# Optimization experiments

Measured on AMD Instinct MI355X. Metric: run time of the kernel, lower is better.

Reference implementation:

```python
import jax, jax.numpy as jnp
import numpy as np

SEQ_LEN = 512
NUM_FEATURES = 16
BATCH = 8
D_MODEL = 512
TOP_K = 5
MAX_P = 512  # largest patch size == seq_len
LAMBD = 0.01


def get_patch_sizes(seq_len):
    # torch: 1/rfftfreq(L)[1:], floor, unique (desc), [::-1] -> ascending unique periods
    freqs = np.fft.rfftfreq(seq_len)[1:]
    periods = np.floor(1.0 / freqs).astype(np.int64)
    return [int(p) for p in np.unique(periods)]


def _sinusoid(n, d):
    pos = np.arange(n, dtype=np.float64)[:, None]
    i = np.arange(d, dtype=np.float64)[None, :]
    angle = pos / np.power(10000.0, (2.0 * np.floor(i / 2.0)) / d)
    return np.where((np.arange(d)[None, :] % 2) == 0, np.sin(angle), np.cos(angle))


def pos_emb_2d(d_model, C, N):
    # 2D sinusoidal positional embedding over (feature idx, patch idx):
    # first half of d_model encodes the feature dim, second half the patch position.
    half = d_model // 2
    pe_feat = _sinusoid(C, half)              # [C, half]
    pe_pos = _sinusoid(N, d_model - half)     # [N, d_model-half]
    pe = np.concatenate([
        np.broadcast_to(pe_feat[:, None, :], (C, N, half)),
        np.broadcast_to(pe_pos[None, :, :], (C, N, d_model - half)),
    ], axis=-1)
    return jnp.asarray(pe, dtype=jnp.float32)  # [C, N, d_model]


def softshrink(x, lambd=LAMBD):
    return jnp.where(x > lambd, x - lambd, jnp.where(x < -lambd, x + lambd, jnp.zeros_like(x)))


def _forward(x, w_start, b_start, w1, b1, w2, b2, w_gate, Wv):
    B, L, C = x.shape
    patch_sizes = get_patch_sizes(L)
    # ---- AFNO1D gating (eval mode: clean logits, no noise) ----
    xs = (x @ w_start)[..., 0] + b_start[0]           # start_fc -> [B, L]
    xf = jnp.fft.rfft(xs, norm='ortho')[:, 1:]        # drop DC -> [B, F], F = L//2
    xr, xi = jnp.real(xf), jnp.imag(xf)
    o1r = jax.nn.relu(xr @ w1[0] - xi @ w1[1] + b1[0])
    o1i = jax.nn.relu(xi @ w1[0] + xr @ w1[1] + b1[1])
    o2r = softshrink(o1r @ w2[0] - o1i @ w2[1] + b2[0])
    o2i = softshrink(o1i @ w2[0] + o1r @ w2[1] + b2[1])
    amp = jnp.sqrt(o2r * o2r + o2i * o2i + 1e-12)     # |complex|, eps for grad safety at 0
    logits = amp @ w_gate                             # [B, E]
    top_w, top_i = jax.lax.top_k(logits, TOP_K)
    top_w = jax.nn.softmax(top_w, axis=-1)
    gates = jnp.zeros_like(logits).at[jnp.arange(B)[:, None], top_i].set(top_w)
    # ---- per-patch-size embedding (dense dispatch: unrouted rows zeroed) ----
    xt = jnp.swapaxes(x, 1, 2)                        # [B, C, L]
    outs = []
    for i, p in enumerate(patch_sizes):               # static loop over 43 experts
        n = -(-L // p)                                # ceil(L / p)
        xp = jnp.pad(xt, ((0, 0), (0, 0), (0, n * p - L)), mode='edge')  # ReplicationPad1d
        patches = xp.reshape(B, C, n, p)              # unfold(-1, p, p)
        emb = jnp.einsum('bcnp,pd->bcnd', patches, Wv[i, :p, :])
        emb = emb + pos_emb_2d(D_MODEL, C, n)[None]
        mask = (gates[:, i] > 0).astype(emb.dtype)
        outs.append(emb * mask[:, None, None, None])
    emb_all = jnp.concatenate(outs, axis=2)           # [B, C, total_patches, d_model]
    return emb_all, gates


def setup_inputs():
    key = jax.random.key(0)
    ks = jax.random.split(key, 8)
    L, C, D = SEQ_LEN, NUM_FEATURES, D_MODEL
    F = L // 2
    E = len(get_patch_sizes(L))
    scale = 1.0 / D
    x = jax.random.normal(ks[0], (BATCH, L, C), jnp.float32)
    w_start = jax.random.normal(ks[1], (C, 1), jnp.float32) / float(np.sqrt(C))
    b_start = jnp.zeros((1,), jnp.float32)
    w1 = scale * jax.random.normal(ks[2], (2, F, 4 * F), jnp.float32)
    b1 = scale * jax.random.normal(ks[3], (2, 4 * F), jnp.float32)
    w2 = scale * jax.random.normal(ks[4], (2, 4 * F, F), jnp.float32)
    b2 = scale * jax.random.normal(ks[5], (2, F), jnp.float32)
    w_gate = 0.01 * jax.random.normal(ks[6], (F, E), jnp.float32)  # randn (not zeros) for nontrivial routing
    Wv = jax.random.normal(ks[7], (E, MAX_P, D), jnp.float32) / float(np.sqrt(MAX_P))  # padded per-expert Linear(p, d_model) weights; expert i uses Wv[i, :p_i]
    return {"x": x, "w_start": w_start, "b_start": b_start, "w1": w1, "b1": b1,
            "w2": w2, "b2": b2, "w_gate": w_gate, "Wv": Wv}


def reference(x, w_start, b_start, w1, b1, w2, b2, w_gate, Wv):
    return _forward(x, w_start, b_start, w1, b1, w2, b2, w_gate, Wv)
```

## Files before the change

### kernel.cpp

```cpp
#include <hip/hip_runtime.h>
#include <math.h>


typedef float v4f __attribute__((ext_vector_type(4)));

constexpr int NEXP = 43;
constexpr int NTOT = 1657;
constexpr long long GATES_OFF = 108593152LL;
constexpr int OUT_V4 = 27148288;

constexpr int WS_XR  = 0;
constexpr int WS_XI  = 2048;
constexpr int WS_O1R = 4096;
constexpr int WS_O1I = 12288;
constexpr int WS_P2  = 20480;
constexpr int WS_PEF = 53248;
constexpr int WS_PEP = 57344;

struct Tables {
  int P[NEXP], N[NEXP], SP[NEXP], G0[NEXP], T0[NEXP+1], TB[5], ne;
};
constexpr int split_of(int p) { return p >= 170 ? 8 : p >= 102 ? 4 : p >= 64 ? 2 : 1; }

constexpr Tables make_tables() {
  Tables t{};
  int ne = 0;
  for (int p = 2; p <= 512; ++p) {
    int k = 512 / p;
    if (k >= 1 && 512 / k == p) t.P[ne++] = p;
  }
  t.ne = ne;
  int g = 0, tl = 0;
  for (int i = 0; i < ne; ++i) {
    int p = t.P[i], n = (512 + p - 1) / p;
    t.N[i] = n; t.SP[i] = split_of(p);
    t.G0[i] = g;  g += n;
    t.T0[i] = tl; tl += n * t.SP[i];
  }
  t.T0[ne] = tl;
  t.TB[0] = 0;
  for (int l = 0; l < 4; ++l) {
    int s = (l == 0) ? 1 : (l == 1) ? 2 : (l == 2) ? 4 : 8;
    int a = 0;
    for (int i = 0; i < ne; ++i) if (t.SP[i] <= s) a += t.N[i] * t.SP[i];
    t.TB[l + 1] = a;
  }
  return t;
}
constexpr Tables HTBL = make_tables();
static_assert(HTBL.ne == 43, "expert count");
static_assert(HTBL.G0[42] + HTBL.N[42] == NTOT, "total patches");
static_assert(HTBL.T0[43] == 1759, "total tiles");
static_assert(HTBL.TB[4] == 1759, "boundaries");

constexpr int NTILE = 1759;
struct TileMap { int v[NTILE]; };
constexpr TileMap make_tmap() {
  TileMap tm{};
  int idx = 0;
  for (int i = 0; i < HTBL.ne; ++i)
    for (int m = 0; m < HTBL.N[i]; ++m)
      for (int cg = 0; cg < HTBL.SP[i]; ++cg)
        tm.v[idx++] = i | (m << 6) | (cg << 15);
  return tm;
}
__constant__ TileMap TMAPC = make_tmap();
__constant__ Tables  TBLC  = make_tables();

__global__ void k_pre(const float* __restrict__ x, const float* __restrict__ w_start,
                      const float* __restrict__ b_start, float* __restrict__ ws) {
  if (blockIdx.x < 8) {
    __shared__ float xs[512];
    int b = blockIdx.x, t = threadIdx.x;
    float w[16];
#pragma unroll
    for (int c = 0; c < 16; ++c) w[c] = w_start[c];
    float bs = b_start[0];
    for (int l = t; l < 512; l += 256) {
      const float* xp = x + ((size_t)b * 512 + l) * 16;
      float s = bs;
#pragma unroll
      for (int c = 0; c < 16; ++c) s = fmaf(xp[c], w[c], s);
      xs[l] = s;
    }
    __syncthreads();
    int k = t + 1;
    float ar = 0.f, ai = 0.f;
    int ph = 0;
    for (int l = 0; l < 512; ++l) {
      float a = (float)ph * (1.0f / 256.0f);
      float v = xs[l];
      ar = fmaf(v,  cospif(a), ar);
      ai = fmaf(-v, sinpif(a), ai);
      ph = (ph + k) & 511;
    }
    const float sc = 0.044194173824159216f;
    ws[WS_XR + b * 256 + t] = ar * sc;
    ws[WS_XI + b * 256 + t] = ai * sc;
  } else {
    int idx = (blockIdx.x - 8) * 256 + threadIdx.x;
    const float K = 0.03597789207803197f;
    if (idx < 4096) {
      int c = idx >> 8, d = idx & 255;
      float ang = (float)c * expf(-(float)(d & ~1) * K);
      ws[WS_PEF + idx] = (d & 1) ? cosf(ang) : sinf(ang);
    } else {
      int r = idx - 4096, mm = r >> 8, j = r & 255;
      float ang = (float)mm * expf(-(float)(j & ~1) * K);
      ws[WS_PEP + r] = (j & 1) ? cosf(ang) : sinf(ang);
    }
  }
}

__global__ void k_fc1(const float* __restrict__ w1, const float* __restrict__ b1,
                      float* __restrict__ ws) {
  __shared__ float xr[256], xi[256];
  int b = blockIdx.x >> 2, jg = blockIdx.x & 3, t = threadIdx.x;
  xr[t] = ws[WS_XR + b * 256 + t];
  xi[t] = ws[WS_XI + b * 256 + t];
  __syncthreads();
  int j = jg * 256 + t;
  float s_ra = 0.f, s_rb = 0.f, s_ia = 0.f, s_ib = 0.f;
  for (int k = 0; k < 256; ++k) {
    float a  = w1[k * 1024 + j];
    float bb = w1[262144 + k * 1024 + j];
    float r = xr[k], im = xi[k];
    s_ra = fmaf(r, a, s_ra);  s_ib = fmaf(im, bb, s_ib);
    s_ia = fmaf(im, a, s_ia); s_rb = fmaf(r, bb, s_rb);
  }
  ws[WS_O1R + b * 1024 + j] = fmaxf(s_ra - s_ib + b1[j], 0.f);
  ws[WS_O1I + b * 1024 + j] = fmaxf(s_ia + s_rb + b1[1024 + j], 0.f);
}

__global__ void k_fc2a(const float* __restrict__ w2, float* __restrict__ ws) {
  __shared__ float lr[256], li[256];
  int b = blockIdx.x >> 2, kc = blockIdx.x & 3, t = threadIdx.x;
  lr[t] = ws[WS_O1R + b * 1024 + kc * 256 + t];
  li[t] = ws[WS_O1I + b * 1024 + kc * 256 + t];
  __syncthreads();
  float s_rr = 0.f, s_ri = 0.f, s_ir = 0.f, s_ii = 0.f;
  int kb = kc * 256;
  for (int k = 0; k < 256; ++k) {
    float a  = w2[(kb + k) * 256 + t];
    float bb = w2[262144 + (kb + k) * 256 + t];
    float r = lr[k], im = li[k];
    s_rr = fmaf(r, a, s_rr);  s_ii = fmaf(im, bb, s_ii);
    s_ir = fmaf(im, a, s_ir); s_ri = fmaf(r, bb, s_ri);
  }
  float* P = ws + WS_P2 + (size_t)(b * 4 + kc) * 1024 + t;
  P[0] = s_rr; P[256] = s_ii; P[512] = s_ir; P[768] = s_ri;
}

__device__ __forceinline__ float softshrink(float v) {
  const float l = 0.01f;
  return v > l ? v - l : (v < -l ? v + l : 0.f);
}

__global__ void k_fc2b(const float* __restrict__ b2, const float* __restrict__ w_gate,
                       float* __restrict__ ws, float* __restrict__ out) {
  __shared__ float amp[256], lg[64];
  int b = blockIdx.x, t = threadIdx.x;
  float s_rr = 0.f, s_ii = 0.f, s_ir = 0.f, s_ri = 0.f;
  for (int kc = 0; kc < 4; ++kc) {
    const float* P = ws + WS_P2 + (size_t)(b * 4 + kc) * 1024 + t;
    s_rr += P[0]; s_ii += P[256]; s_ir += P[512]; s_ri += P[768];
  }
  float o2r = softshrink(s_rr - s_ii + b2[t]);
  float o2i = softshrink(s_ir + s_ri + b2[256 + t]);
  amp[t] = sqrtf(o2r * o2r + o2i * o2i + 1e-12f);
  __syncthreads();
  if (t < NEXP) {
    float s = 0.f;
    for (int k = 0; k < 256; ++k) s = fmaf(amp[k], w_gate[k * NEXP + t], s);
    lg[t] = s;
  }
  __syncthreads();
  if (t == 0) {
    float v[NEXP];
    for (int e = 0; e < NEXP; ++e) v[e] = lg[e];
    float vals[5]; int idx[5];
    for (int r = 0; r < 5; ++r) {
      float best = -INFINITY; int bi = 0;
      for (int e = 0; e < NEXP; ++e)
        if (v[e] > best) { best = v[e]; bi = e; }
      vals[r] = best; idx[r] = bi; v[bi] = -INFINITY;
    }
    float den = 0.f, wv[5];
    for (int r = 0; r < 5; ++r) { wv[r] = expf(vals[r] - vals[0]); den += wv[r]; }
    float g[NEXP];
    for (int e = 0; e < NEXP; ++e) g[e] = 0.f;
    for (int r = 0; r < 5; ++r) g[idx[r]] = wv[r] / den;
    for (int e = 0; e < NEXP; ++e) out[GATES_OFF + (size_t)b * NEXP + e] = g[e];
  }
}

__global__ void k_fill(float* __restrict__ out) {
  size_t id = (size_t)blockIdx.x * 256 + threadIdx.x;
  v4f z = {0.f, 0.f, 0.f, 0.f};
  v4f* o = (v4f*)out;
#pragma unroll
  for (int s = 0; s < 8; ++s)
    o[id + (size_t)s * 3393536] = z;
}

template <int CPG>
__global__ __launch_bounds__(256)
void k_embed(const float* __restrict__ x, const float* __restrict__ Wv,
             const float* __restrict__ ws, float* __restrict__ out, int base) {
  constexpr int CPT = CPG / 2;
  __shared__ __align__(16) float xl[1024];
  int tile = base + blockIdx.x, b = blockIdx.y, t = threadIdx.x;
  int info = TMAPC.v[tile];
  int i = info & 63, m = (info >> 6) & 511, cg = info >> 15;

  float gate = out[GATES_OFF + (size_t)b * NEXP + i];
  if (gate <= 0.f) return;

  int p  = TBLC.P[i];
  int c0 = cg * CPG;
  int g  = TBLC.G0[i] + m;
  int dg = t & 127, tch = t >> 7;
  int d0 = dg * 4;

  int tot = p * CPG;
  for (int id = t; id < tot; id += 256) {
    int q = id / CPG, cc = id % CPG;
    int l = m * p + q; l = l > 511 ? 511 : l;
    xl[id] = x[((size_t)b * 512 + l) * 16 + c0 + cc];
  }
  __syncthreads();

  v4f acc[CPT];
#pragma unroll
  for (int j = 0; j < CPT; ++j) acc[j] = (v4f){0.f, 0.f, 0.f, 0.f};
  const float* wp = Wv + (size_t)i * 262144 + d0;
  const float* xb = xl + tch * CPT;
  for (int q = 0; q < p; ++q) {
    v4f w = *(const v4f*)(wp + (size_t)q * 512);
    const float* xq = xb + q * CPG;
#pragma unroll
    for (int j = 0; j < CPT; ++j) {
      float xv = xq[j];
      acc[j].x = fmaf(xv, w.x, acc[j].x);
      acc[j].y = fmaf(xv, w.y, acc[j].y);
      acc[j].z = fmaf(xv, w.z, acc[j].z);
      acc[j].w = fmaf(xv, w.w, acc[j].w);
    }
  }

  int cA = c0 + tch * CPT;
  const size_t cstride = (size_t)NTOT * 512;
  size_t obase = (((size_t)(b * 16 + cA) * NTOT) + g) * 512 + d0;
  if (d0 < 256) {
#pragma unroll
    for (int j = 0; j < CPT; ++j) {
      v4f pe = *(const v4f*)(ws + WS_PEF + (cA + j) * 256 + d0);
      v4f v = acc[j] + pe;
      *(v4f*)(out + obase + (size_t)j * cstride) = v;
    }
  } else {
    v4f pe = *(const v4f*)(ws + WS_PEP + m * 256 + (d0 - 256));
#pragma unroll
    for (int j = 0; j < CPT; ++j) {
      v4f v = acc[j] + pe;
      *(v4f*)(out + obase + (size_t)j * cstride) = v;
    }
  }
}

extern "C" void kernel_launch(void* const* d_in, const int* in_sizes, int n_in,
                              void* d_out, int out_size, void* d_ws, size_t ws_size,
                              hipStream_t stream) {
  const float* x       = (const float*)d_in[0];
  const float* w_start = (const float*)d_in[1];
  const float* b_start = (const float*)d_in[2];
  const float* w1      = (const float*)d_in[3];
  const float* b1      = (const float*)d_in[4];
  const float* w2      = (const float*)d_in[5];
  const float* b2      = (const float*)d_in[6];
  const float* w_gate  = (const float*)d_in[7];
  const float* Wv      = (const float*)d_in[8];
  float* out = (float*)d_out;
  float* ws  = (float*)d_ws;

  k_pre  <<<280, 256, 0, stream>>>(x, w_start, b_start, ws);
  k_fc1  <<<32,  256, 0, stream>>>(w1, b1, ws);
  k_fc2a <<<32,  256, 0, stream>>>(w2, ws);
  k_fc2b <<<8,   256, 0, stream>>>(b2, w_gate, ws, out);
  k_fill <<<13256, 256, 0, stream>>>(out);

  k_embed<16><<<dim3(HTBL.TB[1], 8), 256, 0, stream>>>(x, Wv, ws, out, 0);
  k_embed<8> <<<dim3(HTBL.TB[2] - HTBL.TB[1], 8), 256, 0, stream>>>(x, Wv, ws, out, HTBL.TB[1]);
  k_embed<4> <<<dim3(HTBL.TB[3] - HTBL.TB[2], 8), 256, 0, stream>>>(x, Wv, ws, out, HTBL.TB[2]);
  k_embed<2> <<<dim3(HTBL.TB[4] - HTBL.TB[3], 8), 256, 0, stream>>>(x, Wv, ws, out, HTBL.TB[3]);
}
```

Baseline: 605.5 us.

## Fuse zero-fill into single embed kernel over patch chunks per batch-channel

Removes the separate full-output zero-fill kernel and the four split-size embed launches, replacing them with one kernel gridded over 16-patch chunks per expert and per (batch, channel). Blocks whose expert gate is zero write zeros for their own slice; active blocks compute the patch projection for one channel. This avoids writing the large output twice, which targets the dominant memory-write cost. In exchange, Wv rows are re-read once per channel instead of being shared across a channel group, and each thread handles one channel with less register reuse.

```diff
diff --git a/kernel.cpp b/kernel.cpp
--- a/kernel.cpp
+++ b/kernel.cpp
@@ -7,7 +7,6 @@
 constexpr int NEXP = 43;
 constexpr int NTOT = 1657;
 constexpr long long GATES_OFF = 108593152LL;
-constexpr int OUT_V4 = 27148288;
 
 constexpr int WS_XR  = 0;
 constexpr int WS_XI  = 2048;
@@ -17,10 +16,7 @@
 constexpr int WS_PEF = 53248;
 constexpr int WS_PEP = 57344;
 
-struct Tables {
-  int P[NEXP], N[NEXP], SP[NEXP], G0[NEXP], T0[NEXP+1], TB[5], ne;
-};
-constexpr int split_of(int p) { return p >= 170 ? 8 : p >= 102 ? 4 : p >= 64 ? 2 : 1; }
+struct Tables { int P[NEXP], N[NEXP], G0[NEXP], ne; };
 
 constexpr Tables make_tables() {
   Tables t{};
@@ -30,42 +26,39 @@
     if (k >= 1 && 512 / k == p) t.P[ne++] = p;
   }
   t.ne = ne;
-  int g = 0, tl = 0;
+  int g = 0;
   for (int i = 0; i < ne; ++i) {
     int p = t.P[i], n = (512 + p - 1) / p;
-    t.N[i] = n; t.SP[i] = split_of(p);
-    t.G0[i] = g;  g += n;
-    t.T0[i] = tl; tl += n * t.SP[i];
-  }
-  t.T0[ne] = tl;
-  t.TB[0] = 0;
-  for (int l = 0; l < 4; ++l) {
-    int s = (l == 0) ? 1 : (l == 1) ? 2 : (l == 2) ? 4 : 8;
-    int a = 0;
-    for (int i = 0; i < ne; ++i) if (t.SP[i] <= s) a += t.N[i] * t.SP[i];
-    t.TB[l + 1] = a;
+    t.N[i] = n; t.G0[i] = g; g += n;
   }
   return t;
 }
 constexpr Tables HTBL = make_tables();
 static_assert(HTBL.ne == 43, "expert count");
 static_assert(HTBL.G0[42] + HTBL.N[42] == NTOT, "total patches");
-static_assert(HTBL.T0[43] == 1759, "total tiles");
-static_assert(HTBL.TB[4] == 1759, "boundaries");
-
-constexpr int NTILE = 1759;
-struct TileMap { int v[NTILE]; };
-constexpr TileMap make_tmap() {
-  TileMap tm{};
-  int idx = 0;
-  for (int i = 0; i < HTBL.ne; ++i)
-    for (int m = 0; m < HTBL.N[i]; ++m)
-      for (int cg = 0; cg < HTBL.SP[i]; ++cg)
-        tm.v[idx++] = i | (m << 6) | (cg << 15);
-  return tm;
-}
-__constant__ TileMap TMAPC = make_tmap();
-__constant__ Tables  TBLC  = make_tables();
+
+constexpr int count_chunks() {
+  int c = 0;
+  for (int i = 0; i < HTBL.ne; ++i) c += (HTBL.N[i] + 15) / 16;
+  return c;
+}
+constexpr int NCHUNK = count_chunks();
+static_assert(NCHUNK == 122, "chunk count");
+
+struct Chunks { int v[NCHUNK]; };
+constexpr Chunks make_chunks() {
+  Chunks c{}; int idx = 0;
+  for (int i = 0; i < HTBL.ne; ++i) {
+    int n = HTBL.N[i];
+    for (int m0 = 0; m0 < n; m0 += 16) {
+      int mc = (n - m0 < 16) ? (n - m0) : 16;
+      c.v[idx++] = i | (m0 << 6) | (mc << 15);
+    }
+  }
+  return c;
+}
+__constant__ Tables TBLC = make_tables();
+__constant__ Chunks CHKC = make_chunks();
 
 __global__ void k_pre(const float* __restrict__ x, const float* __restrict__ w_start,
                       const float* __restrict__ b_start, float* __restrict__ ws) {
@@ -194,77 +187,52 @@
   }
 }
 
-__global__ void k_fill(float* __restrict__ out) {
-  size_t id = (size_t)blockIdx.x * 256 + threadIdx.x;
-  v4f z = {0.f, 0.f, 0.f, 0.f};
-  v4f* o = (v4f*)out;
-#pragma unroll
-  for (int s = 0; s < 8; ++s)
-    o[id + (size_t)s * 3393536] = z;
-}
-
-template <int CPG>
 __global__ __launch_bounds__(256)
-void k_embed(const float* __restrict__ x, const float* __restrict__ Wv,
-             const float* __restrict__ ws, float* __restrict__ out, int base) {
-  constexpr int CPT = CPG / 2;
-  __shared__ __align__(16) float xl[1024];
-  int tile = base + blockIdx.x, b = blockIdx.y, t = threadIdx.x;
-  int info = TMAPC.v[tile];
-  int i = info & 63, m = (info >> 6) & 511, cg = info >> 15;
+void k_main(const float* __restrict__ x, const float* __restrict__ Wv,
+            const float* __restrict__ ws, float* __restrict__ out) {
+  int desc = CHKC.v[blockIdx.x];
+  int i = desc & 63, m0 = (desc >> 6) & 511, mc = desc >> 15;
+  int bc = blockIdx.y, b = bc >> 4, c = bc & 15;
+  int t = threadIdx.x;
 
   float gate = out[GATES_OFF + (size_t)b * NEXP + i];
-  if (gate <= 0.f) return;
-
-  int p  = TBLC.P[i];
-  int c0 = cg * CPG;
-  int g  = TBLC.G0[i] + m;
-  int dg = t & 127, tch = t >> 7;
-  int d0 = dg * 4;
-
-  int tot = p * CPG;
-  for (int id = t; id < tot; id += 256) {
-    int q = id / CPG, cc = id % CPG;
-    int l = m * p + q; l = l > 511 ? 511 : l;
-    xl[id] = x[((size_t)b * 512 + l) * 16 + c0 + cc];
-  }
-  __syncthreads();
-
-  v4f acc[CPT];
-#pragma unroll
-  for (int j = 0; j < CPT; ++j) acc[j] = (v4f){0.f, 0.f, 0.f, 0.f};
+  int g0 = TBLC.G0[i] + m0;
+  size_t base = ((size_t)bc * NTOT + g0) * 512;
+
+  if (gate <= 0.f) {
+    v4f z = {0.f, 0.f, 0.f, 0.f};
+    v4f* o = (v4f*)(out + base);
+    int nv = mc * 128;
+    for (int v = t; v < nv; v += 256) o[v] = z;
+    return;
+  }
+
+  int p = TBLC.P[i];
+  __shared__ float xl[512];
+  for (int l = t; l < 512; l += 256)
+    xl[l] = x[((size_t)b * 512 + l) * 16 + c];
+  __syncthreads();
+
+  int dg = t & 127, d0 = dg * 4, ps = t >> 7;
   const float* wp = Wv + (size_t)i * 262144 + d0;
-  const float* xb = xl + tch * CPT;
-  for (int q = 0; q < p; ++q) {
-    v4f w = *(const v4f*)(wp + (size_t)q * 512);
-    const float* xq = xb + q * CPG;
-#pragma unroll
-    for (int j = 0; j < CPT; ++j) {
-      float xv = xq[j];
-      acc[j].x = fmaf(xv, w.x, acc[j].x);
-      acc[j].y = fmaf(xv, w.y, acc[j].y);
-      acc[j].z = fmaf(xv, w.z, acc[j].z);
-      acc[j].w = fmaf(xv, w.w, acc[j].w);
-    }
-  }
-
-  int cA = c0 + tch * CPT;
-  const size_t cstride = (size_t)NTOT * 512;
-  size_t obase = (((size_t)(b * 16 + cA) * NTOT) + g) * 512 + d0;
-  if (d0 < 256) {
-#pragma unroll
-    for (int j = 0; j < CPT; ++j) {
-      v4f pe = *(const v4f*)(ws + WS_PEF + (cA + j) * 256 + d0);
-      v4f v = acc[j] + pe;
-      *(v4f*)(out + obase + (size_t)j * cstride) = v;
-    }
-  } else {
-    v4f pe = *(const v4f*)(ws + WS_PEP + m * 256 + (d0 - 256));
-#pragma unroll
-    for (int j = 0; j < CPT; ++j) {
-      v4f v = acc[j] + pe;
-      *(v4f*)(out + obase + (size_t)j * cstride) = v;
-    }
+  for (int mm = ps; mm < mc; mm += 2) {
+    int m = m0 + mm;
+    int lb = m * p;
+    v4f acc = {0.f, 0.f, 0.f, 0.f};
+    for (int q = 0; q < p; ++q) {
+      int l = lb + q; l = l > 511 ? 511 : l;
+      float xv = xl[l];
+      v4f w = *(const v4f*)(wp + (size_t)q * 512);
+      acc.x = fmaf(xv, w.x, acc.x);
+      acc.y = fmaf(xv, w.y, acc.y);
+      acc.z = fmaf(xv, w.z, acc.z);
+      acc.w = fmaf(xv, w.w, acc.w);
+    }
+    v4f pe = (d0 < 256)
+      ? *(const v4f*)(ws + WS_PEF + c * 256 + d0)
+      : *(const v4f*)(ws + WS_PEP + m * 256 + (d0 - 256));
+    v4f r = acc + pe;
+    *(v4f*)(out + base + (size_t)mm * 512 + d0) = r;
   }
 }
 
@@ -287,10 +255,5 @@
   k_fc1  <<<32,  256, 0, stream>>>(w1, b1, ws);
   k_fc2a <<<32,  256, 0, stream>>>(w2, ws);
   k_fc2b <<<8,   256, 0, stream>>>(b2, w_gate, ws, out);
-  k_fill <<<13256, 256, 0, stream>>>(out);
-
-  k_embed<16><<<dim3(HTBL.TB[1], 8), 256, 0, stream>>>(x, Wv, ws, out, 0);
-  k_embed<8> <<<dim3(HTBL.TB[2] - HTBL.TB[1], 8), 256, 0, stream>>>(x, Wv, ws, out, HTBL.TB[1]);
-  k_embed<4> <<<dim3(HTBL.TB[3] - HTBL.TB[2], 8), 256, 0, stream>>>(x, Wv, ws, out, HTBL.TB[2]);
-  k_embed<2> <<<dim3(HTBL.TB[4] - HTBL.TB[3], 8), 256, 0, stream>>>(x, Wv, ws, out, HTBL.TB[3]);
-}
+  k_main <<<dim3(NCHUNK, 128), 256, 0, stream>>>(x, Wv, ws, out);
+}
```

Result: faster. 582.1 us (-3.9%).
